# Kernel tuning notes

Measured on AMD Instinct MI355X. Metric: run time of the kernel, lower is better.

Reference implementation:

```python
import jax, jax.numpy as jnp
import numpy as np

K = 27        # num_neighs
EPS = 1e-5    # BatchNorm eps (torch default)
LATENT = 256


def _knn_idx(pts, k):
    # pts: (B, N, 3) -> (B, N, k) indices of k nearest points (self included, dist 0),
    # matching torch_cluster.knn(x, x, k).
    d = jnp.sum((pts[:, :, None, :] - pts[:, None, :, :]) ** 2, axis=-1)  # (B, N, N)
    _, idx = jax.lax.top_k(-d, k)
    return idx


def _graph_feature(x, idx):
    # x: (B, C, N), idx: (B, N, K) -> (B, 2C, N, K) = concat(neigh - center, center)
    xt = jnp.transpose(x, (0, 2, 1))               # (B, N, C)
    neigh = jax.vmap(lambda p, i: p[i])(xt, idx)   # (B, N, K, C) gather
    center = xt[:, :, None, :]                     # (B, N, 1, C)
    feat = jnp.concatenate([neigh - center, jnp.broadcast_to(center, neigh.shape)], axis=-1)
    return jnp.transpose(feat, (0, 3, 1, 2))       # (B, 2C, N, K)


def _bn_lrelu(x, gamma, beta, axes):
    # Training-mode BatchNorm (biased batch stats over `axes`, channel = dim 1) + LeakyReLU(0.2)
    mean = jnp.mean(x, axis=axes, keepdims=True)
    var = jnp.var(x, axis=axes, keepdims=True)
    shape = [1] * x.ndim
    shape[1] = -1
    y = (x - mean) * jax.lax.rsqrt(var + EPS) * gamma.reshape(shape) + beta.reshape(shape)
    return jnp.where(y >= 0, y, 0.2 * y)


def setup_inputs() -> dict:
    key = jax.random.key(0)
    ks = jax.random.split(key, 6)
    B, T, N = 2, 2, 256
    x = jax.random.normal(ks[0], (B, T, N, 3), dtype=jnp.float32)
    # Conv2d(1x1) channel ladder for depth=4, bb_size=24, input_features=6
    dims = [(6, 48), (192, 192), (768, 768), (3072, 3072)]
    inp = {"x": x}
    for i, (cin, cout) in enumerate(dims):
        inp[f"w{i}"] = jax.random.normal(ks[i + 1], (cout, cin), dtype=jnp.float32) * 0.05
        inp[f"g{i}"] = jnp.ones((cout,), jnp.float32)
        inp[f"b{i}"] = jnp.zeros((cout,), jnp.float32)
    # final Conv1d(8160 -> latent): 8160 = 48*(2+8+32+128)
    inp["w4"] = jax.random.normal(ks[5], (LATENT, 8160), dtype=jnp.float32) * 0.02
    inp["g4"] = jnp.ones((LATENT,), jnp.float32)
    inp["b4"] = jnp.zeros((LATENT,), jnp.float32)
    return inp


def reference(x, w0, g0, b0, w1, g1, b1, w2, g2, b2, w3, g3, b3, w4, g4, b4):
    B, T, N, _ = x.shape
    flat = x.reshape(B * T, N, 3)
    idx = _knn_idx(flat, K)  # fixed neighbors reused at every depth (only_true_neighs=True)
    cur = _graph_feature(jnp.transpose(flat, (0, 2, 1)), idx)  # (BT, 6, N, K)
    outs = []
    for w, g, b in [(w0, g0, b0), (w1, g1, b1), (w2, g2, b2), (w3, g3, b3)]:
        if outs:
            cur = _graph_feature(outs[-1], idx)      # (BT, 2C_prev, N, K)
        h = jnp.einsum('bcnk,oc->bonk', cur, w)      # 1x1 conv, no bias
        h = _bn_lrelu(h, g, b, axes=(0, 2, 3))
        hmax = jnp.max(h, axis=-1)                   # max over K neighbors -> (BT, C, N)
        C = hmax.shape[1]
        exp = hmax.reshape(B, T, C, N)
        # Faithful to source: avgpool does `out, _ = x.mean(dim=1, keepdim=True)` which
        # tuple-unpacks the batch dim (requires B==2): out = batch-0 temporal mean (1, C, N),
        # then expanded to (B, T, C, N).
        tp = jnp.mean(exp, axis=1, keepdims=True)[0]  # (1, C, N)
        comb = jnp.concatenate([exp, jnp.broadcast_to(tp[None], exp.shape)], axis=2)  # (B,T,2C,N)
        outs.append(comb.reshape(B * T, 2 * C, N))
    xcat = jnp.concatenate(outs, axis=1)             # (BT, 8160, N)
    y = jnp.einsum('bcn,oc->bon', xcat, w4)          # 1x1 conv1d
    y = _bn_lrelu(y, g4, b4, axes=(0, 2))
    return y.reshape(B, T, LATENT, N)
```

## Files before the change

### kernel.cpp

```cpp
#include <hip/hip_runtime.h>
#include <hip/hip_bf16.h>

#define NPTS 256
#define NB   4
#define KNN  27
#define EPSV 1e-5f

typedef unsigned short u16;
typedef _Float16 f16;
typedef __attribute__((ext_vector_type(8))) _Float16 f16x8;
typedef __attribute__((ext_vector_type(4))) float f32x4;

#define OFF_IDX    0
#define OFF_XYZ    131072
#define OFF_A0     262144
#define OFF_A1     270336
#define OFF_A2     344064
#define OFF_A3     1523712
#define OFF_A4     20398080
#define OFF_PQ     24576000
#define OFF_SLICE  74907648
#define OFF_XC     100073472
#define OFF_Y      116785152

typedef __attribute__((address_space(3))) unsigned int lds_u32_t;
typedef __attribute__((address_space(1))) unsigned int glb_u32_t;

__device__ __forceinline__ void gload16(const f16* g, const u16* l) {
    __builtin_amdgcn_global_load_lds((const glb_u32_t*)g, (lds_u32_t*)(u16*)l, 16, 0, 0);
}

__device__ __forceinline__ float dist3_nocontract(float ax, float ay, float az,
                                                  float bx, float by, float bz) {
#pragma clang fp contract(off)
    float dx = bx - ax, dy = by - ay, dz = bz - az;
    float s = dx * dx;
    s = s + dy * dy;
    s = s + dz * dz;
    return s;
}

__global__ __launch_bounds__(256) void knn_prep(
    const float* __restrict__ x, int* __restrict__ idx, f16* __restrict__ xyz,
    const float* __restrict__ w0, const float* __restrict__ w1,
    const float* __restrict__ w2, const float* __restrict__ w3,
    const float* __restrict__ w4, char* __restrict__ ws)
{
    int bid = blockIdx.x;
    int tid = threadIdx.x;

    if (bid < 1024) {
        if (tid >= 64) return;
        int pt = bid;
        int b = pt >> 8, n = pt & 255;
        int lane = tid;

        float xp0 = x[pt * 3 + 0];
        float xp1 = x[pt * 3 + 1];
        float xp2 = x[pt * 3 + 2];

        if (lane < 32) {
            float v = (lane < 3) ? x[pt * 3 + lane] : 0.f;
            xyz[((long)b * NPTS + n) * 32 + lane] = (f16)v;
        }

        unsigned long long key[4];
#pragma unroll
        for (int u = 0; u < 4; ++u) {
            int j = lane + 64 * u;
            int gj = b * NPTS + j;
            float d = dist3_nocontract(xp0, xp1, xp2,
                                       x[gj * 3 + 0], x[gj * 3 + 1], x[gj * 3 + 2]);
            key[u] = ((unsigned long long)__float_as_uint(d) << 32) | (unsigned int)j;
        }

        for (int r = 0; r < KNN; ++r) {
            unsigned long long m = key[0];
            m = key[1] < m ? key[1] : m;
            m = key[2] < m ? key[2] : m;
            m = key[3] < m ? key[3] : m;
#pragma unroll
            for (int off = 32; off; off >>= 1) {
                unsigned long long o = __shfl_xor(m, off);
                m = o < m ? o : m;
            }
            if (lane == 0) idx[pt * KNN + r] = (int)(m & 0xffffffffu);
#pragma unroll
            for (int u = 0; u < 4; ++u)
                if (key[u] == m) key[u] = ~0ULL;
        }
        return;
    }

    int pbid = bid - 1024;
    const float* w;
    int r, cbase = 0, M, Co, K, Kpad, mode;
    long offA;
    if (pbid < 128)      { w = w0; r = pbid;        M = 96;   Co = 48;   K = 3;    Kpad = 32;   mode = 0; offA = OFF_A0; }
    else if (pbid < 512) { w = w1; r = pbid - 128;  M = 384;  Co = 192;  K = 96;   Kpad = 96;   mode = 0; offA = OFF_A1; }
    else if (pbid < 2048){ w = w2; r = pbid - 512;  M = 1536; Co = 768;  K = 384;  Kpad = 384;  mode = 0; offA = OFF_A2; }
    else if (pbid < 8192){ w = w3; r = pbid - 2048; M = 6144; Co = 3072; K = 1536; Kpad = 1536; mode = 0; offA = OFF_A3; }
    else { int loc = pbid - 8192; w = w4; r = loc >> 2; cbase = (loc & 3) * 2048;
           M = 256; Co = 0; K = 8160; Kpad = 8160; mode = 1; offA = OFF_A4; }

    int c0 = cbase + tid * 8;
    if (c0 >= Kpad) return;
    f16* A = (f16*)(ws + offA);

    f16x8 hv;
#pragma unroll
    for (int j = 0; j < 8; ++j) {
        int c = c0 + j;
        float a = 0.f;
        if (c < K && r < M) {
            if (mode == 1) a = w[(long)r * K + c];
            else if (r < Co) a = w[(long)r * (2 * K) + c];
            else {
                long base = (long)(r - Co) * (2 * K);
                a = w[base + K + c] - w[base + c];
            }
        }
        hv[j] = (f16)a;
    }
    *(f16x8*)&A[(long)r * Kpad + c0] = hv;
}

__global__ __launch_bounds__(256) void gemm_mfma(
    const f16* __restrict__ A, const f16* __restrict__ B,
    float* __restrict__ out, int M, int Kpad, int K,
    int ldF, long bsF, long bsO, int nsplit, long pstride)
{
    __shared__ u16 sA[128 * 32];
    __shared__ u16 sB[128 * 32];

    int bz = blockIdx.z;
    int b = bz / nsplit, slice = bz - b * nsplit;
    int kchunk = (((K + nsplit - 1) / nsplit) + 31) & ~31;
    int kstart = slice * kchunk;
    int kend = K < kstart + kchunk ? K : kstart + kchunk;

    const f16* pB = B + (long)b * bsF;
    float* Ob = out + (long)slice * pstride + (long)b * bsO;

    int m0 = blockIdx.x * 128, n0 = blockIdx.y * 128;
    int tid = threadIdx.x, lane = tid & 63, wid = tid >> 6;
    int wm = (wid >> 1) * 64, wn = (wid & 1) * 64;
    int lrow = lane & 15, quad = lane >> 4;

    int r0 = wid * 16 + (lane >> 2);
    int r1 = 64 + r0;
    int ck = lane & 3;
    int c0 = (ck ^ ((r0 >> 1) & 3)) * 8;
    int c1 = (ck ^ ((r1 >> 1) & 3)) * 8;

    const f16* gA0 = A + (long)(m0 + r0) * Kpad + c0 + kstart;
    const f16* gA1 = A + (long)(m0 + r1) * Kpad + c1 + kstart;
    const f16* gB0 = pB + (long)(n0 + r0) * ldF + c0 + kstart;
    const f16* gB1 = pB + (long)(n0 + r1) * ldF + c1 + kstart;

    const u16* lA0 = &sA[(wid * 16) * 32];
    const u16* lA1 = &sA[(64 + wid * 16) * 32];
    const u16* lB0 = &sB[(wid * 16) * 32];
    const u16* lB1 = &sB[(64 + wid * 16) * 32];

    int fs = (quad ^ ((lrow >> 1) & 3)) * 8;
    int offA = (wm + lrow) * 32 + fs;
    int offB = (wn + lrow) * 32 + fs;

    f32x4 acc[4][4] = {};

    for (int kk = kstart; kk < kend; kk += 32) {
        __syncthreads();
        gload16(gA0, lA0);
        gload16(gA1, lA1);
        gload16(gB0, lB0);
        gload16(gB1, lB1);
        gA0 += 32; gA1 += 32; gB0 += 32; gB1 += 32;
        __syncthreads();

        f16x8 fb[4];
#pragma unroll
        for (int nt = 0; nt < 4; ++nt)
            fb[nt] = *(const f16x8*)&sB[offB + nt * 512];
#pragma unroll
        for (int mt = 0; mt < 4; ++mt) {
            f16x8 fa = *(const f16x8*)&sA[offA + mt * 512];
#pragma unroll
            for (int nt = 0; nt < 4; ++nt)
                acc[mt][nt] = __builtin_amdgcn_mfma_f32_16x16x32_f16(fa, fb[nt], acc[mt][nt], 0, 0, 0);
        }
    }

#pragma unroll
    for (int mt = 0; mt < 4; ++mt)
#pragma unroll
        for (int nt = 0; nt < 4; ++nt) {
            int C = n0 + wn + nt * 16 + lrow;
            int Rb = m0 + wm + mt * 16 + quad * 4;
#pragma unroll
            for (int r = 0; r < 4; ++r) {
                int R = Rb + r;
                if (R < M) Ob[(long)R * NPTS + C] = acc[mt][nt][r];
            }
        }
}

__global__ __launch_bounds__(256) void gather_finalize(
    const float* __restrict__ PQ, long pstride, int nsplit,
    const int* __restrict__ idx,
    const float* __restrict__ g, const float* __restrict__ beta,
    float* __restrict__ slice, int Co)
{
    __shared__ float p_sh[NB][NPTS];
    __shared__ float val_sh[NB][NPTS];
    __shared__ float red[8];
    int o = blockIdx.x;
    int b = threadIdx.x >> 6;
    int lane = threadIdx.x & 63;

    long ip0 = ((long)b * 2 * Co + o) * NPTS;
    long iq0 = ((long)b * 2 * Co + Co + o) * NPTS;

#pragma unroll
    for (int u = 0; u < 4; ++u) {
        int n = lane + 64 * u;
        float v = 0.f;
        for (int s = 0; s < nsplit; ++s) v += PQ[s * pstride + ip0 + n];
        p_sh[b][n] = v;
    }
    __syncthreads();

    float mx[4], mn[4];
    float s = 0.f, ss = 0.f;
#pragma unroll
    for (int u = 0; u < 4; ++u) {
        int n = lane + 64 * u;
        float q = 0.f;
        for (int sp = 0; sp < nsplit; ++sp) q += PQ[sp * pstride + iq0 + n];
        const int* ip = idx + ((long)b * NPTS + n) * KNN;
        float vmx = -__builtin_inff(), vmn = __builtin_inff();
#pragma unroll
        for (int k = 0; k < KNN; ++k) {
            float h = p_sh[b][ip[k]] + q;
            s += h;
            ss += h * h;
            vmx = fmaxf(vmx, h);
            vmn = fminf(vmn, h);
        }
        mx[u] = vmx;
        mn[u] = vmn;
    }
#pragma unroll
    for (int off = 32; off; off >>= 1) {
        s += __shfl_xor(s, off);
        ss += __shfl_xor(ss, off);
    }
    if (lane == 0) { red[b] = s; red[4 + b] = ss; }
    __syncthreads();

    float ts = (red[0] + red[1]) + (red[2] + red[3]);
    float tss = (red[4] + red[5]) + (red[6] + red[7]);
    const float cnt = (float)(NB * NPTS * KNN);
    float mean = ts / cnt;
    float var = tss / cnt - mean * mean;
    float sc = g[o] * (1.0f / sqrtf(var + EPSV));
    float tt = beta[o] - mean * sc;

#pragma unroll
    for (int u = 0; u < 4; ++u) {
        int n = lane + 64 * u;
        float v = (sc >= 0.f) ? mx[u] : mn[u];
        float z = sc * v + tt;
        val_sh[b][n] = z >= 0.f ? z : 0.2f * z;
    }
    __syncthreads();

#pragma unroll
    for (int u = 0; u < 4; ++u) {
        int n = lane + 64 * u;
        float tp = 0.5f * (val_sh[0][n] + val_sh[1][n]);
        slice[((long)b * 2 * Co + o) * NPTS + n] = val_sh[b][n];
        slice[((long)b * 2 * Co + Co + o) * NPTS + n] = tp;
    }
}

__global__ __launch_bounds__(256) void transpose_cn(
    const float* __restrict__ slice, f16* __restrict__ xc,
    int Ctot, int offc)
{
    __shared__ float t[32][33];
    int c0 = blockIdx.x * 32, n0 = blockIdx.y * 32, b = blockIdx.z;
    const float* S = slice + (long)b * Ctot * NPTS;
    int tid = threadIdx.x;
    int r = tid >> 3, s4 = (tid & 7) * 4;

    f32x4 v = *(const f32x4*)&S[(long)(c0 + r) * NPTS + n0 + s4];
    t[r][s4 + 0] = v[0];
    t[r][s4 + 1] = v[1];
    t[r][s4 + 2] = v[2];
    t[r][s4 + 3] = v[3];
    __syncthreads();

    long base = ((long)b * NPTS + n0 + r) * 8160 + offc + c0 + s4;
    typedef __attribute__((ext_vector_type(4))) _Float16 f16x4;
    f16x4 hv;
#pragma unroll
    for (int j = 0; j < 4; ++j) hv[j] = (f16)t[s4 + j][r];
    *(f16x4*)&xc[base] = hv;
}

__global__ __launch_bounds__(256) void final_bn(const float* __restrict__ y,
                                                const float* __restrict__ g4,
                                                const float* __restrict__ b4,
                                                float* __restrict__ out) {
    __shared__ float red[8];
    int o = blockIdx.x;
    int tid = threadIdx.x;
    int lane = tid & 63, w = tid >> 6;

    float v[4];
    float s = 0.f, ss = 0.f;
#pragma unroll
    for (int b = 0; b < 4; ++b) {
        float acc = 0.f;
#pragma unroll
        for (int sp = 0; sp < 16; ++sp)
            acc += y[sp * 262144 + b * 65536 + o * 256 + tid];
        v[b] = acc;
        s += acc;
        ss += acc * acc;
    }
#pragma unroll
    for (int off = 32; off; off >>= 1) {
        s += __shfl_xor(s, off);
        ss += __shfl_xor(ss, off);
    }
    if (lane == 0) { red[w] = s; red[4 + w] = ss; }
    __syncthreads();
    s = (red[0] + red[1]) + (red[2] + red[3]);
    ss = (red[4] + red[5]) + (red[6] + red[7]);
    float mean = s / 1024.f;
    float var = ss / 1024.f - mean * mean;
    float sc = g4[o] * (1.0f / sqrtf(var + EPSV));
    float tt = b4[o] - mean * sc;
#pragma unroll
    for (int b = 0; b < 4; ++b) {
        float z = sc * v[b] + tt;
        z = z >= 0.f ? z : 0.2f * z;
        out[(long)b * 65536 + o * 256 + tid] = z;
    }
}

extern "C" void kernel_launch(void* const* d_in, const int* in_sizes, int n_in,
                              void* d_out, int out_size, void* d_ws, size_t ws_size,
                              hipStream_t stream) {
    const float* x = (const float*)d_in[0];
    const float* wl[4];
    const float* gl[4];
    const float* bl[4];
    for (int i = 0; i < 4; ++i) {
        wl[i] = (const float*)d_in[1 + 3 * i];
        gl[i] = (const float*)d_in[2 + 3 * i];
        bl[i] = (const float*)d_in[3 + 3 * i];
    }
    const float* w4 = (const float*)d_in[13];
    const float* g4 = (const float*)d_in[14];
    const float* b4 = (const float*)d_in[15];

    char* ws = (char*)d_ws;
    int* idx = (int*)(ws + OFF_IDX);
    f16* xyz = (f16*)(ws + OFF_XYZ);
    float* PQ = (float*)(ws + OFF_PQ);
    float* slice = (float*)(ws + OFF_SLICE);
    f16* xc = (f16*)(ws + OFF_XC);
    float* y = (float*)(ws + OFF_Y);

    knn_prep<<<dim3(10240), dim3(256), 0, stream>>>(x, idx, xyz,
                                                    wl[0], wl[1], wl[2], wl[3], w4, ws);

    const int Kp[4] = {32, 96, 384, 1536};
    const int Co[4] = {48, 192, 768, 3072};
    const int offc[4] = {0, 96, 480, 2016};
    const int inoff[4] = {0, 0, 96, 480};
    const int nsp[4] = {1, 3, 4, 2};
    const long aoff[4] = {OFF_A0, OFF_A1, OFF_A2, OFF_A3};

    for (int i = 0; i < 4; ++i) {
        int M = 2 * Co[i];
        int Mpad = (M + 127) & ~127;
        const f16* A = (const f16*)(ws + aoff[i]);

        const f16* Bp;
        int ldF;
        long bsF;
        if (i == 0) { Bp = xyz; ldF = 32; bsF = (long)NPTS * 32; }
        else { Bp = xc + inoff[i]; ldF = 8160; bsF = (long)NPTS * 8160; }

        long pstride = (long)NB * M * NPTS;
        gemm_mfma<<<dim3(Mpad / 128, NPTS / 128, NB * nsp[i]), dim3(256), 0, stream>>>(
            A, Bp, PQ, M, Kp[i], Kp[i], ldF, bsF, (long)M * NPTS, nsp[i], pstride);

        gather_finalize<<<dim3(Co[i]), dim3(256), 0, stream>>>(
            PQ, pstride, nsp[i], idx, gl[i], bl[i], slice, Co[i]);
        transpose_cn<<<dim3(M / 32, NPTS / 32, NB), dim3(256), 0, stream>>>(
            slice, xc, M, offc[i]);
    }

    gemm_mfma<<<dim3(2, 2, NB * 16), dim3(256), 0, stream>>>(
        (const f16*)(ws + OFF_A4), xc, y, 256, 8160, 8160, 8160,
        (long)NPTS * 8160, (long)256 * NPTS, 16, (long)NB * 256 * NPTS);
    final_bn<<<dim3(256), dim3(256), 0, stream>>>(y, g4, b4, (float*)d_out);
}
```

Measured before the change: 303.9 us.

## Restructure weight prep, interleave KNN blocks, pad idx, store slice in fp16

The prep kernel now builds both halves of each weight row (center part and neighbor difference) from one set of vectorized loads, which cuts the block count. KNN blocks are interleaved with prep blocks, and neighbor indices are padded to 28 so they can be read as int4. gather_finalize factors the per-neighbor BN statistics so q is added once per point, and it writes the intermediate slice in fp16. The transpose kernel then moves half-width data. The risks are slight fp16 rounding in the slice, which was already converted to fp16 at transpose, and algebraic reassociation of the variance sums.

```diff
diff --git a/kernel.cpp b/kernel.cpp
--- a/kernel.cpp
+++ b/kernel.cpp
@@ -9,6 +9,7 @@
 typedef unsigned short u16;
 typedef _Float16 f16;
 typedef __attribute__((ext_vector_type(8))) _Float16 f16x8;
+typedef __attribute__((ext_vector_type(4))) _Float16 f16x4;
 typedef __attribute__((ext_vector_type(4))) float f32x4;
 
 #define OFF_IDX    0
@@ -49,9 +50,9 @@
     int bid = blockIdx.x;
     int tid = threadIdx.x;
 
-    if (bid < 1024) {
+    if (bid < 4096 && (bid & 3) == 3) {
         if (tid >= 64) return;
-        int pt = bid;
+        int pt = bid >> 2;
         int b = pt >> 8, n = pt & 255;
         int lane = tid;
 
@@ -84,7 +85,7 @@
                 unsigned long long o = __shfl_xor(m, off);
                 m = o < m ? o : m;
             }
-            if (lane == 0) idx[pt * KNN + r] = (int)(m & 0xffffffffu);
+            if (lane == 0) idx[pt * 28 + r] = (int)(m & 0xffffffffu);
 #pragma unroll
             for (int u = 0; u < 4; ++u)
                 if (key[u] == m) key[u] = ~0ULL;
@@ -92,37 +93,110 @@
         return;
     }
 
-    int pbid = bid - 1024;
-    const float* w;
-    int r, cbase = 0, M, Co, K, Kpad, mode;
-    long offA;
-    if (pbid < 128)      { w = w0; r = pbid;        M = 96;   Co = 48;   K = 3;    Kpad = 32;   mode = 0; offA = OFF_A0; }
-    else if (pbid < 512) { w = w1; r = pbid - 128;  M = 384;  Co = 192;  K = 96;   Kpad = 96;   mode = 0; offA = OFF_A1; }
-    else if (pbid < 2048){ w = w2; r = pbid - 512;  M = 1536; Co = 768;  K = 384;  Kpad = 384;  mode = 0; offA = OFF_A2; }
-    else if (pbid < 8192){ w = w3; r = pbid - 2048; M = 6144; Co = 3072; K = 1536; Kpad = 1536; mode = 0; offA = OFF_A3; }
-    else { int loc = pbid - 8192; w = w4; r = loc >> 2; cbase = (loc & 3) * 2048;
-           M = 256; Co = 0; K = 8160; Kpad = 8160; mode = 1; offA = OFF_A4; }
-
-    int c0 = cbase + tid * 8;
-    if (c0 >= Kpad) return;
-    f16* A = (f16*)(ws + offA);
-
-    f16x8 hv;
-#pragma unroll
-    for (int j = 0; j < 8; ++j) {
-        int c = c0 + j;
-        float a = 0.f;
-        if (c < K && r < M) {
-            if (mode == 1) a = w[(long)r * K + c];
-            else if (r < Co) a = w[(long)r * (2 * K) + c];
-            else {
-                long base = (long)(r - Co) * (2 * K);
-                a = w[base + K + c] - w[base + c];
+    int pbid = (bid < 4096) ? (bid - (bid >> 2)) : (bid - 1024);
+
+    if (pbid == 0) {
+        f16* A = (f16*)(ws + OFF_A0);
+        int jj = tid >> 2;
+        int cc = (tid & 3) * 8;
+        if (jj < 48) {
+            f16x8 lo = {}, df = {};
+#pragma unroll
+            for (int j = 0; j < 8; ++j) {
+                int c = cc + j;
+                if (c < 3) {
+                    float a = w0[jj * 6 + c];
+                    float b2 = w0[jj * 6 + 3 + c];
+                    lo[j] = (f16)a;
+                    df[j] = (f16)(b2 - a);
+                }
             }
-        }
-        hv[j] = (f16)a;
-    }
-    *(f16x8*)&A[(long)r * Kpad + c0] = hv;
+            *(f16x8*)&A[jj * 32 + cc] = lo;
+            *(f16x8*)&A[(48 + jj) * 32 + cc] = df;
+        }
+        if (jj < 32) {
+            f16x8 z = {};
+            *(f16x8*)&A[(96 + jj) * 32 + cc] = z;
+        }
+        return;
+    }
+    if (pbid < 13) {
+        f16* A = (f16*)(ws + OFF_A1);
+        int j = (pbid - 1) * 16 + (tid >> 4);
+        int cc = (tid & 15) * 8;
+        if (cc >= 96) return;
+        f32x4 a0 = *(const f32x4*)&w1[j * 192 + cc];
+        f32x4 a1 = *(const f32x4*)&w1[j * 192 + cc + 4];
+        f32x4 b0 = *(const f32x4*)&w1[j * 192 + 96 + cc];
+        f32x4 b1 = *(const f32x4*)&w1[j * 192 + 96 + cc + 4];
+        f16x8 lo, df;
+#pragma unroll
+        for (int j2 = 0; j2 < 4; ++j2) {
+            lo[j2] = (f16)a0[j2];     lo[4 + j2] = (f16)a1[j2];
+            df[j2] = (f16)(b0[j2] - a0[j2]);
+            df[4 + j2] = (f16)(b1[j2] - a1[j2]);
+        }
+        *(f16x8*)&A[j * 96 + cc] = lo;
+        *(f16x8*)&A[(192 + j) * 96 + cc] = df;
+        return;
+    }
+    if (pbid < 205) {
+        f16* A = (f16*)(ws + OFF_A2);
+        int j = (pbid - 13) * 4 + (tid >> 6);
+        int cc = (tid & 63) * 8;
+        if (cc >= 384) return;
+        f32x4 a0 = *(const f32x4*)&w2[(long)j * 768 + cc];
+        f32x4 a1 = *(const f32x4*)&w2[(long)j * 768 + cc + 4];
+        f32x4 b0 = *(const f32x4*)&w2[(long)j * 768 + 384 + cc];
+        f32x4 b1 = *(const f32x4*)&w2[(long)j * 768 + 384 + cc + 4];
+        f16x8 lo, df;
+#pragma unroll
+        for (int j2 = 0; j2 < 4; ++j2) {
+            lo[j2] = (f16)a0[j2];     lo[4 + j2] = (f16)a1[j2];
+            df[j2] = (f16)(b0[j2] - a0[j2]);
+            df[4 + j2] = (f16)(b1[j2] - a1[j2]);
+        }
+        *(f16x8*)&A[(long)j * 384 + cc] = lo;
+        *(f16x8*)&A[(long)(768 + j) * 384 + cc] = df;
+        return;
+    }
+    if (pbid < 3277) {
+        f16* A = (f16*)(ws + OFF_A3);
+        int j = pbid - 205;
+        int cc = tid * 8;
+        if (cc >= 1536) return;
+        f32x4 a0 = *(const f32x4*)&w3[(long)j * 3072 + cc];
+        f32x4 a1 = *(const f32x4*)&w3[(long)j * 3072 + cc + 4];
+        f32x4 b0 = *(const f32x4*)&w3[(long)j * 3072 + 1536 + cc];
+        f32x4 b1 = *(const f32x4*)&w3[(long)j * 3072 + 1536 + cc + 4];
+        f16x8 lo, df;
+#pragma unroll
+        for (int j2 = 0; j2 < 4; ++j2) {
+            lo[j2] = (f16)a0[j2];     lo[4 + j2] = (f16)a1[j2];
+            df[j2] = (f16)(b0[j2] - a0[j2]);
+            df[4 + j2] = (f16)(b1[j2] - a1[j2]);
+        }
+        *(f16x8*)&A[(long)j * 1536 + cc] = lo;
+        *(f16x8*)&A[(long)(3072 + j) * 1536 + cc] = df;
+        return;
+    }
+    {
+        f16* A = (f16*)(ws + OFF_A4);
+        int loc = pbid - 3277;
+        int r = loc >> 2;
+        int c0 = (loc & 3) * 2048 + tid * 8;
+        if (c0 >= 8160) return;
+        f32x4 a0 = *(const f32x4*)&w4[(long)r * 8160 + c0];
+        f32x4 a1 = *(const f32x4*)&w4[(long)r * 8160 + c0 + 4];
+        f16x8 hv;
+#pragma unroll
+        for (int j2 = 0; j2 < 4; ++j2) {
+            hv[j2] = (f16)a0[j2];
+            hv[4 + j2] = (f16)a1[j2];
+        }
+        *(f16x8*)&A[(long)r * 8160 + c0] = hv;
+        return;
+    }
 }
 
 __global__ __launch_bounds__(256) void gemm_mfma(
@@ -209,7 +283,7 @@
     const float* __restrict__ PQ, long pstride, int nsplit,
     const int* __restrict__ idx,
     const float* __restrict__ g, const float* __restrict__ beta,
-    float* __restrict__ slice, int Co)
+    f16* __restrict__ slice, int Co)
 {
     __shared__ float p_sh[NB][NPTS];
     __shared__ float val_sh[NB][NPTS];
@@ -236,19 +310,31 @@
     for (int u = 0; u < 4; ++u) {
         int n = lane + 64 * u;
         float q = 0.f;
-        for (int sp = 0; sp < nsplit; ++sp) q += PQ[sp * pstride + iq0 + n];
-        const int* ip = idx + ((long)b * NPTS + n) * KNN;
-        float vmx = -__builtin_inff(), vmn = __builtin_inff();
+        for (int sp2 = 0; sp2 < nsplit; ++sp2) q += PQ[sp2 * pstride + iq0 + n];
+
+        const int4* ip4 = (const int4*)(idx + ((long)b * NPTS + n) * 28);
+        int nb[28];
+#pragma unroll
+        for (int w = 0; w < 7; ++w) {
+            int4 t = ip4[w];
+            nb[4 * w] = t.x; nb[4 * w + 1] = t.y;
+            nb[4 * w + 2] = t.z; nb[4 * w + 3] = t.w;
+        }
+
+        float sp = 0.f, spp = 0.f;
+        float pmx = -__builtin_inff(), pmn = __builtin_inff();
 #pragma unroll
         for (int k = 0; k < KNN; ++k) {
-            float h = p_sh[b][ip[k]] + q;
-            s += h;
-            ss += h * h;
-            vmx = fmaxf(vmx, h);
-            vmn = fminf(vmn, h);
-        }
-        mx[u] = vmx;
-        mn[u] = vmn;
+            float p = p_sh[b][nb[k]];
+            sp += p;
+            spp = fmaf(p, p, spp);
+            pmx = fmaxf(pmx, p);
+            pmn = fminf(pmn, p);
+        }
+        s += sp + 27.f * q;
+        ss += spp + q * fmaf(2.f, sp, 27.f * q);
+        mx[u] = pmx + q;
+        mn[u] = pmn + q;
     }
 #pragma unroll
     for (int off = 32; off; off >>= 1) {
@@ -279,33 +365,33 @@
     for (int u = 0; u < 4; ++u) {
         int n = lane + 64 * u;
         float tp = 0.5f * (val_sh[0][n] + val_sh[1][n]);
-        slice[((long)b * 2 * Co + o) * NPTS + n] = val_sh[b][n];
-        slice[((long)b * 2 * Co + Co + o) * NPTS + n] = tp;
+        slice[((long)b * 2 * Co + o) * NPTS + n] = (f16)val_sh[b][n];
+        slice[((long)b * 2 * Co + Co + o) * NPTS + n] = (f16)tp;
     }
 }
 
 __global__ __launch_bounds__(256) void transpose_cn(
-    const float* __restrict__ slice, f16* __restrict__ xc,
+    const f16* __restrict__ slice, f16* __restrict__ xc,
     int Ctot, int offc)
 {
-    __shared__ float t[32][33];
+    __shared__ u16 t[32][36];
     int c0 = blockIdx.x * 32, n0 = blockIdx.y * 32, b = blockIdx.z;
-    const float* S = slice + (long)b * Ctot * NPTS;
+    const f16* S = slice + (long)b * Ctot * NPTS;
     int tid = threadIdx.x;
     int r = tid >> 3, s4 = (tid & 7) * 4;
 
-    f32x4 v = *(const f32x4*)&S[(long)(c0 + r) * NPTS + n0 + s4];
-    t[r][s4 + 0] = v[0];
-    t[r][s4 + 1] = v[1];
-    t[r][s4 + 2] = v[2];
-    t[r][s4 + 3] = v[3];
+    f16x4 v = *(const f16x4*)&S[(long)(c0 + r) * NPTS + n0 + s4];
+    t[r][s4 + 0] = ((const u16*)&v)[0];
+    t[r][s4 + 1] = ((const u16*)&v)[1];
+    t[r][s4 + 2] = ((const u16*)&v)[2];
+    t[r][s4 + 3] = ((const u16*)&v)[3];
     __syncthreads();
 
     long base = ((long)b * NPTS + n0 + r) * 8160 + offc + c0 + s4;
-    typedef __attribute__((ext_vector_type(4))) _Float16 f16x4;
     f16x4 hv;
-#pragma unroll
-    for (int j = 0; j < 4; ++j) hv[j] = (f16)t[s4 + j][r];
+    u16* hp = (u16*)&hv;
+#pragma unroll
+    for (int j = 0; j < 4; ++j) hp[j] = t[s4 + j][r];
     *(f16x4*)&xc[base] = hv;
 }
 
@@ -371,12 +457,12 @@
     int* idx = (int*)(ws + OFF_IDX);
     f16* xyz = (f16*)(ws + OFF_XYZ);
     float* PQ = (float*)(ws + OFF_PQ);
-    float* slice = (float*)(ws + OFF_SLICE);
+    f16* slice = (f16*)(ws + OFF_SLICE);
     f16* xc = (f16*)(ws + OFF_XC);
     float* y = (float*)(ws + OFF_Y);
 
-    knn_prep<<<dim3(10240), dim3(256), 0, stream>>>(x, idx, xyz,
-                                                    wl[0], wl[1], wl[2], wl[3], w4, ws);
+    knn_prep<<<dim3(5325), dim3(256), 0, stream>>>(x, idx, xyz,
+                                                   wl[0], wl[1], wl[2], wl[3], w4, ws);
 
     const int Kp[4] = {32, 96, 384, 1536};
     const int Co[4] = {48, 192, 768, 3072};
```

Measured after the change: 289.0 us. 1.05x faster.
